# Performance work log

Measured on AMD Instinct MI355X. Metric: run time of the kernel, lower is better.

Reference implementation:

```python
import jax, jax.numpy as jnp
import numpy as np

NUM_Q_HEADS = 16
NUM_KV_HEADS = 4
GROUP_SIZE = NUM_Q_HEADS // NUM_KV_HEADS  # 4
GROUP_DIM = 128                           # head dim, also RoPE dim
THETA = 10000.0


def _rope_cos_sin(num_tokens, dim, dtype):
    # freqs = 1/theta^(2i/d); angles[t, i] = t * freqs[i]
    inv_freq = 1.0 / (THETA ** (jnp.arange(0, dim, 2, dtype=jnp.float32) / dim))
    t = jnp.arange(num_tokens, dtype=jnp.float32)
    angles = jnp.outer(t, inv_freq)  # [N, d/2]
    # broadcast to [N, 1, 1, d/2] to match q/k shape [B, N, gs, kvh, d/2]
    cos = jnp.cos(angles)[:, None, None, :].astype(dtype)
    sin = jnp.sin(angles)[:, None, None, :].astype(dtype)
    return cos, sin


def _apply_rope(x, cos, sin):
    # x: [B, N, gs, kvh, d]; complex rotation on interleaved (even, odd) pairs
    xr = x.reshape(*x.shape[:-1], -1, 2)
    xe, xo = xr[..., 0], xr[..., 1]
    oe = xe * cos - xo * sin
    oo = xe * sin + xo * cos
    return jnp.stack([oe, oo], axis=-1).reshape(x.shape)


def setup_inputs() -> dict:
    key = jax.random.key(0)
    ks = jax.random.split(key, 5)
    B, N, D = 1, 2048, 2048
    KV_D = GROUP_DIM * NUM_KV_HEADS  # 512
    s = 0.02
    return {
        "x": jax.random.normal(ks[0], (B, N, D), dtype=jnp.float32),
        "Wq": jax.random.normal(ks[1], (D, D), dtype=jnp.float32) * s,
        "Wk": jax.random.normal(ks[2], (D, KV_D), dtype=jnp.float32) * s,
        "Wv": jax.random.normal(ks[3], (D, KV_D), dtype=jnp.float32) * s,
        "Wo": jax.random.normal(ks[4], (D, D), dtype=jnp.float32) * s,
    }


def reference(x, Wq, Wk, Wv, Wo):
    B, N, D = x.shape
    d = GROUP_DIM
    # projections
    q = (x @ Wq).reshape(B, N, GROUP_SIZE, NUM_KV_HEADS, d)
    k = (x @ Wk).reshape(B, N, 1, NUM_KV_HEADS, d)
    v = (x @ Wv).reshape(B, N, 1, NUM_KV_HEADS, d)
    # RoPE (interleaved complex rotation)
    cos, sin = _rope_cos_sin(N, d, x.dtype)
    q = _apply_rope(q, cos, sin)
    k = _apply_rope(k, cos, sin)
    # to [B, kvh, gs, N, d] / [B, kvh, N, d]
    q = jnp.transpose(q, (0, 3, 2, 1, 4))        # b k s n d
    k = jnp.transpose(k[:, :, 0], (0, 2, 1, 3))  # b k m d
    v = jnp.transpose(v[:, :, 0], (0, 2, 1, 3))  # b k m d
    scores = jnp.einsum('bksnd,bkmd->bksnm', q, k)
    causal = jnp.tril(jnp.ones((N, N), dtype=bool))
    scores = jnp.where(causal, scores, -jnp.inf)
    weights = jax.nn.softmax(scores / jnp.sqrt(jnp.asarray(d, x.dtype)), axis=-1)
    ctx = jnp.einsum('bksnm,bkmd->bksnd', weights, v)   # [B, kvh, gs, N, d]
    # flatten heads (kvh-major, matching torch flatten(1,2)), then [B, N, D]
    ctx = ctx.reshape(B, NUM_KV_HEADS * GROUP_SIZE, N, d)
    ctx = jnp.transpose(ctx, (0, 2, 1, 3)).reshape(B, N, D)
    return ctx @ Wo
```

## Files before the change

### kernel.cpp

```cpp
#include <hip/hip_runtime.h>

typedef unsigned short u16;
typedef float f32x4 __attribute__((ext_vector_type(4)));
typedef short s16x8 __attribute__((ext_vector_type(8)));
typedef short s16x4 __attribute__((ext_vector_type(4)));

__device__ __forceinline__ u16 f2b(float f) {
  union { float f; unsigned u; } v; v.f = f;
  unsigned r = v.u + 0x7fffu + ((v.u >> 16) & 1u);
  return (u16)(r >> 16);
}
__device__ __forceinline__ float b2f(u16 b) {
  union { unsigned u; float f; } v; v.u = ((unsigned)b) << 16;
  return v.f;
}
__device__ __forceinline__ f32x4 mfma_bf16(s16x8 a, s16x8 b, f32x4 c) {
  return __builtin_amdgcn_mfma_f32_16x16x32_bf16(a, b, c, 0, 0, 0);
}
__device__ __forceinline__ void gl_lds16(const u16* g, u16* l) {
  __builtin_amdgcn_global_load_lds(
      (const __attribute__((address_space(1))) void*)g,
      (__attribute__((address_space(3))) void*)l, 16, 0, 0);
}

__global__ void conv_x(const float* __restrict__ in, u16* __restrict__ out, int n) {
  int i = (blockIdx.x * 256 + threadIdx.x) * 8;
  if (i >= n) return;
  f32x4 a = *(const f32x4*)(in + i);
  f32x4 b = *(const f32x4*)(in + i + 4);
  s16x8 o = {(short)f2b(a.x), (short)f2b(a.y), (short)f2b(a.z), (short)f2b(a.w),
             (short)f2b(b.x), (short)f2b(b.y), (short)f2b(b.z), (short)f2b(b.w)};
  *(s16x8*)(out + i) = o;
}

__global__ void transW_qkv(const float* __restrict__ Wq, const float* __restrict__ Wk,
                           const float* __restrict__ Wv, u16* __restrict__ WqkvT) {
  __shared__ u16 tile[64][68];
  const int ox = blockIdx.x * 64;
  const int oy = blockIdx.y * 64;
  const float* src; int scol, C;
  if (ox < 2048)      { src = Wq; scol = ox;        C = 2048; }
  else if (ox < 2560) { src = Wk; scol = ox - 2048; C = 512;  }
  else                { src = Wv; scol = ox - 2560; C = 512;  }
  const int t = threadIdx.x, lr = t >> 4, c4 = (t & 15) * 4;
#pragma unroll
  for (int p = 0; p < 4; ++p) {
    int r = p * 16 + lr;
    f32x4 v = *(const f32x4*)(src + (size_t)(oy + r) * C + scol + c4);
    s16x4 pk = {(short)f2b(v.x), (short)f2b(v.y), (short)f2b(v.z), (short)f2b(v.w)};
    *(s16x4*)(&tile[r][c4]) = pk;
  }
  __syncthreads();
#pragma unroll
  for (int q = 0; q < 4; ++q) {
    int oc = q * 16 + lr;
    s16x4 pk = {(short)tile[c4 + 0][oc], (short)tile[c4 + 1][oc],
                (short)tile[c4 + 2][oc], (short)tile[c4 + 3][oc]};
    *(s16x4*)(WqkvT + (size_t)(ox + oc) * 2048 + oy + c4) = pk;
  }
}

__global__ void transW_o(const float* __restrict__ Wo, u16* __restrict__ WoT) {
  __shared__ u16 tile[64][68];
  const int ox = blockIdx.x * 64, oy = blockIdx.y * 64;
  const int t = threadIdx.x, lr = t >> 4, c4 = (t & 15) * 4;
#pragma unroll
  for (int p = 0; p < 4; ++p) {
    int r = p * 16 + lr;
    f32x4 v = *(const f32x4*)(Wo + (size_t)(oy + r) * 2048 + ox + c4);
    s16x4 pk = {(short)f2b(v.x), (short)f2b(v.y), (short)f2b(v.z), (short)f2b(v.w)};
    *(s16x4*)(&tile[r][c4]) = pk;
  }
  __syncthreads();
#pragma unroll
  for (int q = 0; q < 4; ++q) {
    int oc = q * 16 + lr;
    s16x4 pk = {(short)tile[c4 + 0][oc], (short)tile[c4 + 1][oc],
                (short)tile[c4 + 2][oc], (short)tile[c4 + 3][oc]};
    *(s16x4*)(WoT + (size_t)(ox + oc) * 2048 + oy + c4) = pk;
  }
}

__global__ void transpose_v(const u16* __restrict__ qkv, u16* __restrict__ vT) {
  __shared__ u16 tile[64][68];
  const int bx = blockIdx.x * 64, by = blockIdx.y * 64;
  const int t = threadIdx.x, lr = t >> 4, c4 = (t & 15) * 4;
#pragma unroll
  for (int p = 0; p < 4; ++p) {
    int r = p * 16 + lr;
    s16x4 v = *(const s16x4*)(qkv + (size_t)(by + r) * 3072 + 2560 + bx + c4);
    *(s16x4*)(&tile[r][c4]) = v;
  }
  __syncthreads();
#pragma unroll
  for (int q = 0; q < 4; ++q) {
    int oc = q * 16 + lr;
    s16x4 pk = {(short)tile[c4 + 0][oc], (short)tile[c4 + 1][oc],
                (short)tile[c4 + 2][oc], (short)tile[c4 + 3][oc]};
    *(s16x4*)(vT + (size_t)(bx + oc) * 2048 + by + c4) = pk;
  }
}

__device__ __forceinline__ void gemm_core(const u16* __restrict__ A,
                                          const u16* __restrict__ Bt,
                                          int kbeg, int kend, int K,
                                          int m0, int n0,
                                          f32x4 (*acc)[4], u16* As, u16* Bs) {
  const int t = threadIdx.x;
  const int wave = t >> 6, lane = t & 63, quad = lane >> 4, lc = lane & 15;
  const int wm = (wave >> 1) * 64, wn = (wave & 1) * 64;
  for (int k0 = kbeg; k0 < kend; k0 += 32) {
#pragma unroll
    for (int h = 0; h < 2; ++h) {
      int ch = h * 256 + t, row = ch >> 2, kc = (ch & 3) * 8;
      gl_lds16(A  + (size_t)(m0 + row) * K + k0 + kc, As + (size_t)(h * 256 + wave * 64) * 8);
      gl_lds16(Bt + (size_t)(n0 + row) * K + k0 + kc, Bs + (size_t)(h * 256 + wave * 64) * 8);
    }
    __syncthreads();
    s16x8 af[4], bfr[4];
#pragma unroll
    for (int i = 0; i < 4; ++i)
      af[i] = *(const s16x8*)(As + (wm + i * 16 + lc) * 32 + quad * 8);
#pragma unroll
    for (int j = 0; j < 4; ++j)
      bfr[j] = *(const s16x8*)(Bs + (wn + j * 16 + lc) * 32 + quad * 8);
#pragma unroll
    for (int i = 0; i < 4; ++i)
#pragma unroll
      for (int j = 0; j < 4; ++j)
        acc[i][j] = mfma_bf16(af[i], bfr[j], acc[i][j]);
    __syncthreads();
  }
}

__global__ __launch_bounds__(256, 2) void gemm_qkv_half(const u16* __restrict__ A,
                                                        const u16* __restrict__ Bt,
                                                        u16* __restrict__ P) {
  __shared__ __align__(16) u16 As[128 * 32];
  __shared__ __align__(16) u16 Bs[128 * 32];
  const int kh = blockIdx.z;
  const int n0 = blockIdx.x * 128, m0 = blockIdx.y * 128;
  const int lane = threadIdx.x & 63, wave = threadIdx.x >> 6;
  const int quad = lane >> 4, lc = lane & 15;
  const int wm = (wave >> 1) * 64, wn = (wave & 1) * 64;
  const f32x4 z = {0.f, 0.f, 0.f, 0.f};
  f32x4 acc[4][4];
#pragma unroll
  for (int i = 0; i < 4; ++i)
#pragma unroll
    for (int j = 0; j < 4; ++j) acc[i][j] = z;
  gemm_core(A, Bt, kh * 1024, kh * 1024 + 1024, 2048, m0, n0, acc, As, Bs);
  u16* Pk = P + (size_t)kh * (2048 * 3072);
#pragma unroll
  for (int i = 0; i < 4; ++i)
#pragma unroll
    for (int j = 0; j < 4; ++j)
#pragma unroll
      for (int r = 0; r < 4; ++r)
        Pk[(size_t)(m0 + wm + i * 16 + quad * 4 + r) * 3072 + n0 + wn + j * 16 + lc] =
            f2b(acc[i][j][r]);
}

__global__ void reduce_rope(const u16* __restrict__ P, u16* __restrict__ qkv) {
  const int lin = blockIdx.x * 256 + threadIdx.x;
  const int row = lin / 384, c8 = (lin - row * 384) * 8;
  const u16* p0 = P + (size_t)row * 3072 + c8;
  s16x8 a = *(const s16x8*)p0;
  s16x8 b = *(const s16x8*)(p0 + 6291456);
  float v[8];
#pragma unroll
  for (int i = 0; i < 8; ++i) v[i] = b2f((u16)a[i]) + b2f((u16)b[i]);
  if (c8 < 2560) {
#pragma unroll
    for (int h = 0; h < 4; ++h) {
      const int i = 2 * h;
      const int ip = ((c8 + i) & 127) >> 1;
      const float ang = (float)row * exp2f(-0.20762050593046014f * (float)ip);
      float sv, cv;
      sincosf(ang, &sv, &cv);
      const float e = v[i], o = v[i + 1];
      v[i]     = e * cv - o * sv;
      v[i + 1] = e * sv + o * cv;
    }
  }
  s16x8 o;
#pragma unroll
  for (int i = 0; i < 8; ++i) o[i] = (short)f2b(v[i]);
  *(s16x8*)(qkv + (size_t)row * 3072 + c8) = o;
}

__global__ __launch_bounds__(256, 2) void gemm_out_half(const u16* __restrict__ A,
                                                        const u16* __restrict__ Bt,
                                                        u16* __restrict__ Po) {
  __shared__ __align__(16) u16 As[128 * 32];
  __shared__ __align__(16) u16 Bs[128 * 32];
  const int kh = blockIdx.z;
  const int n0 = blockIdx.x * 128, m0 = blockIdx.y * 128;
  const int lane = threadIdx.x & 63, wave = threadIdx.x >> 6;
  const int quad = lane >> 4, lc = lane & 15;
  const int wm = (wave >> 1) * 64, wn = (wave & 1) * 64;
  const f32x4 z = {0.f, 0.f, 0.f, 0.f};
  f32x4 acc[4][4];
#pragma unroll
  for (int i = 0; i < 4; ++i)
#pragma unroll
    for (int j = 0; j < 4; ++j) acc[i][j] = z;
  gemm_core(A, Bt, kh * 1024, kh * 1024 + 1024, 2048, m0, n0, acc, As, Bs);
  u16* Pk = Po + (size_t)kh * (2048 * 2048);
#pragma unroll
  for (int i = 0; i < 4; ++i)
#pragma unroll
    for (int j = 0; j < 4; ++j)
#pragma unroll
      for (int r = 0; r < 4; ++r)
        Pk[(size_t)(m0 + wm + i * 16 + quad * 4 + r) * 2048 + n0 + wn + j * 16 + lc] =
            f2b(acc[i][j][r]);
}

__global__ void reduce_out(const u16* __restrict__ Po, float* __restrict__ out) {
  const int lin = blockIdx.x * 256 + threadIdx.x;
  const u16* p0 = Po + (size_t)lin * 8;
  s16x8 a = *(const s16x8*)p0;
  s16x8 b = *(const s16x8*)(p0 + 4194304);
  f32x4 o0, o1;
#pragma unroll
  for (int i = 0; i < 4; ++i) o0[i] = b2f((u16)a[i]) + b2f((u16)b[i]);
#pragma unroll
  for (int i = 0; i < 4; ++i) o1[i] = b2f((u16)a[i + 4]) + b2f((u16)b[i + 4]);
  *(f32x4*)(out + (size_t)lin * 8) = o0;
  *(f32x4*)(out + (size_t)lin * 8 + 4) = o1;
}

__global__ __launch_bounds__(256, 2) void attn_k(const u16* __restrict__ qkv,
                                                 const u16* __restrict__ vT,
                                                 u16* __restrict__ Opart,
                                                 float* __restrict__ Lpart) {
  const int bid = blockIdx.x;
  const int hq = bid / 40, idx = bid % 40;
  int qt, c;
  if (idx < 4)       { qt = idx;                          c = 0; }
  else if (idx < 12) { int w = idx - 4;  qt = 4 + (w >> 1);  c = w & 1; }
  else if (idx < 24) { int w = idx - 12; qt = 8 + w / 3;     c = w % 3; }
  else               { int w = idx - 24; qt = 12 + (w >> 2); c = w & 3; }
  const int s0 = c * 8;
  const int s1 = min(c * 8 + 8, 2 * qt + 2);

  const int kvh = hq & 3;
  const int qc0 = hq << 7, kc0 = 2048 + (kvh << 7), vr0 = kvh << 7;

  __shared__ __align__(16) u16 Ks[64 * 136];
  __shared__ __align__(16) u16 Vs[128 * 72];
  __shared__ __align__(16) u16 Ps[128 * 72];

  const int t = threadIdx.x, wave = t >> 6, lane = t & 63;
  const int quad = lane >> 4, lc = lane & 15;
  const int kr = t >> 4, kc = (t & 15) * 8;
  const int vr = t >> 3, vc = (t & 7) * 8;

  s16x8 qf[2][4];
#pragma unroll
  for (int i = 0; i < 2; ++i)
#pragma unroll
    for (int ks = 0; ks < 4; ++ks)
      qf[i][ks] = *(const s16x8*)(qkv +
          (size_t)(qt * 128 + wave * 32 + i * 16 + lc) * 3072 +
          qc0 + ks * 32 + quad * 8);

  const f32x4 z = {0.f, 0.f, 0.f, 0.f};
  f32x4 oa[2][8];
#pragma unroll
  for (int i = 0; i < 2; ++i)
#pragma unroll
    for (int n = 0; n < 8; ++n) oa[i][n] = z;
  float Ls[2][4] = {{0.f, 0.f, 0.f, 0.f}, {0.f, 0.f, 0.f, 0.f}};
  const float scale2 = 0.12751744545f;

  s16x8 kpf[4], vpf[4];
  {
    const int j0 = s0 * 64;
#pragma unroll
    for (int p = 0; p < 4; ++p)
      kpf[p] = *(const s16x8*)(qkv + (size_t)(j0 + p * 16 + kr) * 3072 + kc0 + kc);
#pragma unroll
    for (int p = 0; p < 4; ++p)
      vpf[p] = *(const s16x8*)(vT + (size_t)(vr0 + p * 32 + vr) * 2048 + j0 + vc);
  }

  for (int tile = s0; tile < s1; ++tile) {
    const int j0 = tile * 64;
    __syncthreads();
#pragma unroll
    for (int p = 0; p < 4; ++p)
      *(s16x8*)(Ks + (p * 16 + kr) * 136 + kc) = kpf[p];
#pragma unroll
    for (int p = 0; p < 4; ++p)
      *(s16x8*)(Vs + (p * 32 + vr) * 72 + vc) = vpf[p];
    __syncthreads();
    if (tile + 1 < s1) {
      const int j1 = j0 + 64;
#pragma unroll
      for (int p = 0; p < 4; ++p)
        kpf[p] = *(const s16x8*)(qkv + (size_t)(j1 + p * 16 + kr) * 3072 + kc0 + kc);
#pragma unroll
      for (int p = 0; p < 4; ++p)
        vpf[p] = *(const s16x8*)(vT + (size_t)(vr0 + p * 32 + vr) * 2048 + j1 + vc);
    }
    f32x4 sa[2][4];
#pragma unroll
    for (int i = 0; i < 2; ++i)
#pragma unroll
      for (int n = 0; n < 4; ++n) sa[i][n] = z;
    __builtin_amdgcn_s_setprio(1);
#pragma unroll
    for (int ks = 0; ks < 4; ++ks)
#pragma unroll
      for (int n = 0; n < 4; ++n) {
        s16x8 bf = *(const s16x8*)(Ks + (n * 16 + lc) * 136 + ks * 32 + quad * 8);
        sa[0][n] = mfma_bf16(qf[0][ks], bf, sa[0][n]);
        sa[1][n] = mfma_bf16(qf[1][ks], bf, sa[1][n]);
      }
    __builtin_amdgcn_s_setprio(0);
#pragma unroll
    for (int i = 0; i < 2; ++i) {
      const int qrow_base = qt * 128 + wave * 32 + i * 16 + quad * 4;
#pragma unroll
      for (int n = 0; n < 4; ++n) {
        int jc = j0 + n * 16 + lc;
#pragma unroll
        for (int r = 0; r < 4; ++r) {
          float e = (jc <= qrow_base + r) ? exp2f(sa[i][n][r] * scale2) : 0.f;
          Ps[(wave * 32 + i * 16 + quad * 4 + r) * 72 + n * 16 + lc] = f2b(e);
          Ls[i][r] += e;
        }
      }
    }
    __builtin_amdgcn_s_setprio(1);
#pragma unroll
    for (int ks = 0; ks < 2; ++ks)
#pragma unroll
      for (int i = 0; i < 2; ++i) {
        s16x8 af = *(const s16x8*)(Ps + (wave * 32 + i * 16 + lc) * 72 +
                                   ks * 32 + quad * 8);
#pragma unroll
        for (int n = 0; n < 8; ++n) {
          s16x8 bf = *(const s16x8*)(Vs + (n * 16 + lc) * 72 + ks * 32 + quad * 8);
          oa[i][n] = mfma_bf16(af, bf, oa[i][n]);
        }
      }
    __builtin_amdgcn_s_setprio(0);
  }
#pragma unroll
  for (int i = 0; i < 2; ++i)
#pragma unroll
    for (int r = 0; r < 4; ++r) {
      float s = Ls[i][r];
      s += __shfl_xor(s, 1);
      s += __shfl_xor(s, 2);
      s += __shfl_xor(s, 4);
      s += __shfl_xor(s, 8);
      Ls[i][r] = s;
    }
  u16* Ob = Opart + (size_t)bid * (128 * 128);
  if (lc == 0) {
#pragma unroll
    for (int i = 0; i < 2; ++i)
#pragma unroll
      for (int r = 0; r < 4; ++r)
        Lpart[(size_t)bid * 128 + wave * 32 + i * 16 + quad * 4 + r] = Ls[i][r];
  }
#pragma unroll
  for (int i = 0; i < 2; ++i)
#pragma unroll
    for (int n = 0; n < 8; ++n)
#pragma unroll
      for (int r = 0; r < 4; ++r)
        Ob[(wave * 32 + i * 16 + quad * 4 + r) * 128 + n * 16 + lc] =
            f2b(oa[i][n][r]);
}

__global__ void attn_combine(const u16* __restrict__ Opart,
                             const float* __restrict__ Lpart,
                             u16* __restrict__ ctx) {
  const int hq = blockIdx.y, kvh = hq & 3, sg = hq >> 2;
  const int lin = blockIdx.x * 256 + threadIdx.x;
  const int token = lin >> 4, d8 = (lin & 15) << 3;
  const int qt = token >> 7, row = token & 127;
  const int tier = qt >> 2;
  const int btab[4] = {0, 4, 12, 24};
  const int base = hq * 40 + btab[tier] + (qt & 3) * (tier + 1);
  const int cnt = tier + 1;
  float acc[8] = {0.f, 0.f, 0.f, 0.f, 0.f, 0.f, 0.f, 0.f};
  float L = 0.f;
  for (int c = 0; c < cnt; ++c) {
    const int b = base + c;
    L += Lpart[(size_t)b * 128 + row];
    s16x8 o = *(const s16x8*)(Opart + (size_t)b * 16384 + row * 128 + d8);
#pragma unroll
    for (int i = 0; i < 8; ++i) acc[i] += b2f((u16)o[i]);
  }
  const float inv = 1.f / L;
  s16x8 out;
#pragma unroll
  for (int i = 0; i < 8; ++i) out[i] = (short)f2b(acc[i] * inv);
  *(s16x8*)(ctx + (size_t)token * 2048 + ((kvh * 4 + sg) << 7) + d8) = out;
}

extern "C" void kernel_launch(void* const* d_in, const int* in_sizes, int n_in,
                              void* d_out, int out_size, void* d_ws, size_t ws_size,
                              hipStream_t stream) {
  const float* x  = (const float*)d_in[0];
  const float* Wq = (const float*)d_in[1];
  const float* Wk = (const float*)d_in[2];
  const float* Wv = (const float*)d_in[3];
  const float* Wo = (const float*)d_in[4];

  char* base = (char*)d_ws;
  u16*   xb    = (u16*)(base);
  u16*   qkvb  = (u16*)(base);
  u16*   WoT   = (u16*)(base);
  u16*   WqkvT = (u16*)(base + 8388608);
  u16*   vTb   = (u16*)(base + 12582912);
  float* Lpart = (float*)(base + 14680064);
  u16*   Pq    = (u16*)(base + 20971520);
  u16*   Opart = (u16*)(base + 20971520);
  u16*   Po    = (u16*)(base + 20971520);
  u16*   ctxb  = (u16*)(base + 41943040);

  conv_x<<<2048, 256, 0, stream>>>(x, xb, 2048 * 2048);
  transW_qkv<<<dim3(48, 32), 256, 0, stream>>>(Wq, Wk, Wv, WqkvT);

  gemm_qkv_half<<<dim3(24, 16, 2), 256, 0, stream>>>(xb, WqkvT, Pq);
  reduce_rope<<<3072, 256, 0, stream>>>(Pq, qkvb);

  transpose_v<<<dim3(8, 32), 256, 0, stream>>>(qkvb, vTb);

  attn_k<<<640, 256, 0, stream>>>(qkvb, vTb, Opart, Lpart);
  attn_combine<<<dim3(128, 16), 256, 0, stream>>>(Opart, Lpart, ctxb);

  transW_o<<<dim3(32, 32), 256, 0, stream>>>(Wo, WoT);
  gemm_out_half<<<dim3(16, 16, 2), 256, 0, stream>>>(ctxb, WoT, Po);
  reduce_out<<<2048, 256, 0, stream>>>(Po, (float*)d_out);
}
```

Before: 239.5 us.

## Drop split-K in QKV GEMM and fuse RoPE into its epilogue

Runs the QKV projection GEMM over the full K range in one pass, with no split-K halves. RoPE is applied directly on the accumulators, using a lane shuffle to fetch each even/odd pair partner. This removes the bf16 partial-sum buffer write and read and the separate reduce_rope launch. The workspace layout is reshuffled so buffers stay disjoint. The trade-off is half as many GEMM blocks, which lowers parallelism, plus per-element sincos in the epilogue.

```diff
diff --git a/kernel.cpp b/kernel.cpp
--- a/kernel.cpp
+++ b/kernel.cpp
@@ -133,12 +133,11 @@
   }
 }
 
-__global__ __launch_bounds__(256, 2) void gemm_qkv_half(const u16* __restrict__ A,
+__global__ __launch_bounds__(256, 2) void gemm_qkv_rope(const u16* __restrict__ A,
                                                         const u16* __restrict__ Bt,
-                                                        u16* __restrict__ P) {
+                                                        u16* __restrict__ qkv) {
   __shared__ __align__(16) u16 As[128 * 32];
   __shared__ __align__(16) u16 Bs[128 * 32];
-  const int kh = blockIdx.z;
   const int n0 = blockIdx.x * 128, m0 = blockIdx.y * 128;
   const int lane = threadIdx.x & 63, wave = threadIdx.x >> 6;
   const int quad = lane >> 4, lc = lane & 15;
@@ -149,44 +148,38 @@
   for (int i = 0; i < 4; ++i)
 #pragma unroll
     for (int j = 0; j < 4; ++j) acc[i][j] = z;
-  gemm_core(A, Bt, kh * 1024, kh * 1024 + 1024, 2048, m0, n0, acc, As, Bs);
-  u16* Pk = P + (size_t)kh * (2048 * 3072);
-#pragma unroll
-  for (int i = 0; i < 4; ++i)
-#pragma unroll
-    for (int j = 0; j < 4; ++j)
-#pragma unroll
-      for (int r = 0; r < 4; ++r)
-        Pk[(size_t)(m0 + wm + i * 16 + quad * 4 + r) * 3072 + n0 + wn + j * 16 + lc] =
-            f2b(acc[i][j][r]);
-}
-
-__global__ void reduce_rope(const u16* __restrict__ P, u16* __restrict__ qkv) {
-  const int lin = blockIdx.x * 256 + threadIdx.x;
-  const int row = lin / 384, c8 = (lin - row * 384) * 8;
-  const u16* p0 = P + (size_t)row * 3072 + c8;
-  s16x8 a = *(const s16x8*)p0;
-  s16x8 b = *(const s16x8*)(p0 + 6291456);
-  float v[8];
-#pragma unroll
-  for (int i = 0; i < 8; ++i) v[i] = b2f((u16)a[i]) + b2f((u16)b[i]);
-  if (c8 < 2560) {
-#pragma unroll
-    for (int h = 0; h < 4; ++h) {
-      const int i = 2 * h;
-      const int ip = ((c8 + i) & 127) >> 1;
-      const float ang = (float)row * exp2f(-0.20762050593046014f * (float)ip);
-      float sv, cv;
-      sincosf(ang, &sv, &cv);
-      const float e = v[i], o = v[i + 1];
-      v[i]     = e * cv - o * sv;
-      v[i + 1] = e * sv + o * cv;
+  gemm_core(A, Bt, 0, 2048, 2048, m0, n0, acc, As, Bs);
+
+  if (n0 < 2560) {
+    const float sgn = (lc & 1) ? 1.f : -1.f;
+#pragma unroll
+    for (int j = 0; j < 4; ++j) {
+      const int col = n0 + wn + j * 16 + lc;
+      const int ip = (col & 127) >> 1;
+      const float freq = exp2f(-0.20762050593046014f * (float)ip);
+#pragma unroll
+      for (int i = 0; i < 4; ++i)
+#pragma unroll
+        for (int r = 0; r < 4; ++r) {
+          const int row = m0 + wm + i * 16 + quad * 4 + r;
+          float v = acc[i][j][r];
+          float w = __shfl_xor(v, 1);
+          float sv, cv;
+          sincosf((float)row * freq, &sv, &cv);
+          float res = fmaf(v, cv, sgn * w * sv);
+          qkv[(size_t)row * 3072 + col] = f2b(res);
+        }
     }
-  }
-  s16x8 o;
-#pragma unroll
-  for (int i = 0; i < 8; ++i) o[i] = (short)f2b(v[i]);
-  *(s16x8*)(qkv + (size_t)row * 3072 + c8) = o;
+  } else {
+#pragma unroll
+    for (int i = 0; i < 4; ++i)
+#pragma unroll
+      for (int j = 0; j < 4; ++j)
+#pragma unroll
+        for (int r = 0; r < 4; ++r)
+          qkv[(size_t)(m0 + wm + i * 16 + quad * 4 + r) * 3072 +
+              n0 + wn + j * 16 + lc] = f2b(acc[i][j][r]);
+  }
 }
 
 __global__ __launch_bounds__(256, 2) void gemm_out_half(const u16* __restrict__ A,
@@ -416,21 +409,19 @@
 
   char* base = (char*)d_ws;
   u16*   xb    = (u16*)(base);
-  u16*   qkvb  = (u16*)(base);
-  u16*   WoT   = (u16*)(base);
   u16*   WqkvT = (u16*)(base + 8388608);
-  u16*   vTb   = (u16*)(base + 12582912);
-  float* Lpart = (float*)(base + 14680064);
-  u16*   Pq    = (u16*)(base + 20971520);
-  u16*   Opart = (u16*)(base + 20971520);
-  u16*   Po    = (u16*)(base + 20971520);
-  u16*   ctxb  = (u16*)(base + 41943040);
+  u16*   qkvb  = (u16*)(base + 20971520);
+  u16*   vTb   = (u16*)(base + 33554432);
+  float* Lpart = (float*)(base + 35651584);
+  u16*   ctxb  = (u16*)(base + 35979264);
+  u16*   Opart = (u16*)(base);
+  u16*   WoT   = (u16*)(base + 20971520);
+  u16*   Po    = (u16*)(base);
 
   conv_x<<<2048, 256, 0, stream>>>(x, xb, 2048 * 2048);
   transW_qkv<<<dim3(48, 32), 256, 0, stream>>>(Wq, Wk, Wv, WqkvT);
 
-  gemm_qkv_half<<<dim3(24, 16, 2), 256, 0, stream>>>(xb, WqkvT, Pq);
-  reduce_rope<<<3072, 256, 0, stream>>>(Pq, qkvb);
+  gemm_qkv_rope<<<dim3(24, 16), 256, 0, stream>>>(xb, WqkvT, qkvb);
 
   transpose_v<<<dim3(8, 32), 256, 0, stream>>>(qkvb, vTb);
 
```

Result: slower. 718.9 us (+200.2%).
